# Kernel tuning notes

Hardware: AMD Instinct MI355X
Metric: run time of the kernel (lower is better)

## Reference

```python
import jax, jax.numpy as jnp
import numpy as np

EPS = 1e-7  # K.epsilon()


def setup_inputs() -> dict:
    key = jax.random.key(0)
    k1, k2, k3 = jax.random.split(key, 3)
    B, T, D = 32, 2048, 1024
    one = jax.random.normal(k1, (B, D), dtype=jnp.float32)
    many = jax.random.normal(k2, (B, T, D), dtype=jnp.float32)
    W = jax.random.normal(k3, (D, D), dtype=jnp.float32) * (1.0 / np.sqrt(D))
    return {"one": one, "many": many, "W": W}


def reference(one, many, W):
    # logits = batch_dot(tanh(many @ W), one, axes=[2,1]) -> [B, T]
    proj = jnp.tanh(jnp.einsum('btd,de->bte', many, W))       # [B,T,D]
    logits = jnp.einsum('btd,bd->bt', proj, one)               # [B,T]
    # stable softmax with Keras epsilon in denominator
    ai = jnp.exp(logits - jnp.max(logits, axis=-1, keepdims=True))
    att_weights = ai / (jnp.sum(ai, axis=-1, keepdims=True) + EPS)  # [B,T]
    result = jnp.einsum('btd,bt->bd', many, att_weights)       # [B,D]
    return result, att_weights
```

## Files before the change

kernel.cpp:

```cpp
#include <hip/hip_runtime.h>
#include <hip/hip_bf16.h>

typedef _Float16 half8v __attribute__((ext_vector_type(8)));
typedef __fp16  fp16x2 __attribute__((ext_vector_type(2)));
typedef float floatx4 __attribute__((ext_vector_type(4)));

#define NB 32
#define NT 2048
#define ND 1024
#define NM (NB * NT)

#define GL16(g, l)                                                             \
    __builtin_amdgcn_global_load_lds(                                          \
        (const __attribute__((address_space(1))) void*)(g),                    \
        (__attribute__((address_space(3))) void*)(l), 16, 0, 0)

__device__ __forceinline__ float fast_tanh(float x) {
    x = fminf(9.0f, fmaxf(-9.0f, x));
    float e = __builtin_amdgcn_exp2f(x * 2.8853900817779268f);
    return (e - 1.0f) * __builtin_amdgcn_rcpf(e + 1.0f);
}

__global__ __launch_bounds__(256)
void wt_kernel(const float* __restrict__ W, _Float16* __restrict__ Wt) {
    __shared__ float tile[32][33];
    int tx = threadIdx.x, ty = threadIdx.y;
    int bx = blockIdx.x, by = blockIdx.y;
    #pragma unroll
    for (int i = 0; i < 4; ++i) {
        int y = by * 32 + ty + i * 8;
        tile[ty + i * 8][tx] = W[y * ND + bx * 32 + tx];
    }
    __syncthreads();
    #pragma unroll
    for (int i = 0; i < 4; ++i) {
        int e = bx * 32 + ty + i * 8;
        Wt[e * ND + by * 32 + tx] = (_Float16)tile[tx][ty + i * 8];
    }
}

__global__ __launch_bounds__(256)
void conv_kernel(const float* __restrict__ many, _Float16* __restrict__ manyh) {
    size_t idx = ((size_t)blockIdx.x * 256 + threadIdx.x) * 8;
    size_t stride = (size_t)gridDim.x * 256 * 8;
    for (size_t i = idx; i < (size_t)NM * ND; i += stride) {
        float4 a = *reinterpret_cast<const float4*>(many + i);
        float4 b = *reinterpret_cast<const float4*>(many + i + 4);
        union { _Float16 h[8]; uint4 u; } o;
        o.h[0] = (_Float16)a.x; o.h[1] = (_Float16)a.y;
        o.h[2] = (_Float16)a.z; o.h[3] = (_Float16)a.w;
        o.h[4] = (_Float16)b.x; o.h[5] = (_Float16)b.y;
        o.h[6] = (_Float16)b.z; o.h[7] = (_Float16)b.w;
        *reinterpret_cast<uint4*>(manyh + i) = o.u;
    }
}

__global__ __launch_bounds__(512, 2)
void gemm_logits_8p(const _Float16* __restrict__ manyh, const _Float16* __restrict__ Wt,
                    const float* __restrict__ one, float* __restrict__ logits) {
    __shared__ uint4 LDSQ[8192];
    char* Ld = (char*)LDSQ;

    int bid = blockIdx.x;
    int j = (bid & 7) * 128 + (bid >> 3);
    int mb = j >> 2, nb = j & 3;
    int m0 = mb * 256, n0 = nb * 256;

    int tid = threadIdx.x;
    int lane = tid & 63, w = tid >> 6;
    int wr = w >> 2, wc = w & 3;
    int l15 = lane & 15, l4 = lane >> 4;

    const char* aS = (const char*)manyh + ((size_t)(m0 + (tid >> 3)) << 11)
                   + (size_t)(((tid & 7) ^ ((tid >> 3) & 7)) << 4);
    const char* bS = (const char*)Wt + ((size_t)(n0 + (tid >> 3)) << 11)
                   + (size_t)(((tid & 7) ^ ((tid >> 3) & 7)) << 4);
    int ldst = tid * 16;

#define SU(OP, H, L, TT)                                                        \
    GL16(((OP) ? bS : aS) + (((size_t)((H) * 128 + (L) * 64)) << 11) + (TT) * 128, \
         Ld + (((TT) & 1) << 16) + ((OP) << 15) + ((H) << 14) + ((L) << 13) + ldst)

    floatx4 acc[8][4] = {};
    int key = l15 & 7;
    int lofA0 = l15 * 128 + (((0 | l4) ^ key) << 4);
    int lofA1 = l15 * 128 + (((4 | l4) ^ key) << 4);

    SU(0, 0, 0, 0); SU(0, 1, 0, 0);
    SU(0, 0, 1, 0); SU(0, 1, 1, 0);
    SU(1, 0, 0, 0); SU(1, 0, 1, 0);
    SU(1, 1, 0, 0); SU(1, 1, 1, 0);
    SU(0, 0, 0, 1); SU(0, 1, 0, 1);
    asm volatile("s_waitcnt vmcnt(2)" ::: "memory");
    __builtin_amdgcn_sched_barrier(0);
    __builtin_amdgcn_s_barrier();

    #pragma unroll 1
    for (int t = 0; t < 16; ++t) {
        const char* ab = Ld + ((t & 1) << 16) + (wr << 14);
        const char* bb = Ld + ((t & 1) << 16) + 32768 + ((wc >> 1) << 14)
                       + ((wc & 1) << 13);
        half8v bf0[4], bf1[4];
        #pragma unroll
        for (int p = 0; p < 4; ++p) {
            int rb = (p * 32) << 7;
            half8v a0k0 = *(const half8v*)(ab + rb + lofA0);
            half8v a0k1 = *(const half8v*)(ab + rb + lofA1);
            half8v a1k0 = *(const half8v*)(ab + rb + (16 << 7) + lofA0);
            half8v a1k1 = *(const half8v*)(ab + rb + (16 << 7) + lofA1);
            if (p == 0) {
                #pragma unroll
                for (int ni = 0; ni < 4; ++ni) {
                    bf0[ni] = *(const half8v*)(bb + ((ni * 16) << 7) + lofA0);
                    bf1[ni] = *(const half8v*)(bb + ((ni * 16) << 7) + lofA1);
                }
            }
            if (t < 15) {
                if (p == 0)      { SU(0, 0, 1, t + 1); SU(0, 1, 1, t + 1); }
                else if (p == 1) { SU(1, 0, 0, t + 1); SU(1, 0, 1, t + 1); }
                else if (p == 2) { SU(1, 1, 0, t + 1); SU(1, 1, 1, t + 1); }
                else if (t < 14) { SU(0, 0, 0, t + 2); SU(0, 1, 0, t + 2); }
            }
            __builtin_amdgcn_s_barrier();
            __builtin_amdgcn_s_setprio(1);
            #pragma unroll
            for (int ni = 0; ni < 4; ++ni) {
                acc[2 * p][ni] = __builtin_amdgcn_mfma_f32_16x16x32_f16(
                    a0k0, bf0[ni], acc[2 * p][ni], 0, 0, 0);
                acc[2 * p][ni] = __builtin_amdgcn_mfma_f32_16x16x32_f16(
                    a0k1, bf1[ni], acc[2 * p][ni], 0, 0, 0);
                acc[2 * p + 1][ni] = __builtin_amdgcn_mfma_f32_16x16x32_f16(
                    a1k0, bf0[ni], acc[2 * p + 1][ni], 0, 0, 0);
                acc[2 * p + 1][ni] = __builtin_amdgcn_mfma_f32_16x16x32_f16(
                    a1k1, bf1[ni], acc[2 * p + 1][ni], 0, 0, 0);
            }
            __builtin_amdgcn_s_setprio(0);
            if (p == 3) {
                if (t < 14)       asm volatile("s_waitcnt vmcnt(2)" ::: "memory");
                else if (t == 14) asm volatile("s_waitcnt vmcnt(0)" ::: "memory");
                __builtin_amdgcn_sched_barrier(0);
            }
            __builtin_amdgcn_s_barrier();
        }
    }
#undef SU

    int bidx = m0 >> 11;
    float onev[4];
    #pragma unroll
    for (int ni = 0; ni < 4; ++ni)
        onev[ni] = one[(bidx << 10) + n0 + wc * 64 + ni * 16 + l15];

    #pragma unroll
    for (int mi = 0; mi < 8; ++mi) {
        float part[4] = {0.f, 0.f, 0.f, 0.f};
        #pragma unroll
        for (int ni = 0; ni < 4; ++ni)
            #pragma unroll
            for (int b = 0; b < 4; ++b)
                part[b] += fast_tanh(acc[mi][ni][b]) * onev[ni];
        #pragma unroll
        for (int off = 1; off < 16; off <<= 1)
            #pragma unroll
            for (int b = 0; b < 4; ++b)
                part[b] += __shfl_xor(part[b], off, 64);
        #pragma unroll
        for (int b = 0; b < 4; ++b)
            if (l15 == ((mi * 4 + b) & 15))
                atomicAdd(&logits[m0 + wr * 128 + mi * 16 + l4 * 4 + b], part[b]);
    }
}

__global__ __launch_bounds__(256, 2)
void gemm_logits(const float* __restrict__ many, const _Float16* __restrict__ Wt,
                 const float* __restrict__ one, float* __restrict__ logits) {
    __shared__ uint4 AsQ[2048];
    __shared__ uint4 BsQ[1024];
    char* AsB = (char*)AsQ;
    char* BsB = (char*)BsQ;

    int bid = blockIdx.x;
    int j = (bid & 7) * 512 + (bid >> 3);
    int mb = j >> 3, nb = j & 7;
    int m0 = mb * 128, n0 = nb * 128;

    int tid = threadIdx.x;
    int lane = tid & 63, w = tid >> 6;
    int wr = w >> 1, wc = w & 1;
    int l15 = lane & 15, l4 = lane >> 4;

    const char* aS = (const char*)many + ((size_t)(m0 + (tid >> 4)) << 12)
        + (size_t)(((tid & 15) ^ ((tid >> 4) & 7)) << 4);
    const char* bS = (const char*)Wt + ((size_t)(n0 + (tid >> 3)) << 11)
        + (size_t)(((tid & 7) ^ ((tid >> 3) & 7)) << 4);
    char* aD = AsB + tid * 16;
    char* bD = BsB + tid * 16;

    floatx4 acc[4][4] = {};

    for (int kb = 0; kb < 1024; kb += 64) {
        #pragma unroll
        for (int i = 0; i < 8; ++i)
            GL16(aS + kb * 4 + i * 65536, aD + i * 4096);
        #pragma unroll
        for (int i = 0; i < 4; ++i)
            GL16(bS + kb * 2 + i * 65536, bD + i * 4096);
        __syncthreads();

        #pragma unroll
        for (int ks = 0; ks < 64; ks += 32) {
            half8v af[4], bf[4];
            #pragma unroll
            for (int mi = 0; mi < 4; ++mi) {
                int r = wr * 64 + mi * 16 + l15;
                int s = l15 & 7;
                const char* base = AsB + r * 256;
                int c0 = (ks >> 2) + l4 * 2;
                float4 x = *(const float4*)(base + (size_t)((c0 ^ s) << 4));
                float4 y = *(const float4*)(base + (size_t)(((c0 + 1) ^ s) << 4));
                union { fp16x2 p[4]; half8v h; } u;
                u.p[0] = __builtin_amdgcn_cvt_pkrtz(x.x, x.y);
                u.p[1] = __builtin_amdgcn_cvt_pkrtz(x.z, x.w);
                u.p[2] = __builtin_amdgcn_cvt_pkrtz(y.x, y.y);
                u.p[3] = __builtin_amdgcn_cvt_pkrtz(y.z, y.w);
                af[mi] = u.h;
            }
            #pragma unroll
            for (int ni = 0; ni < 4; ++ni) {
                int r = wc * 64 + ni * 16 + l15;
                int s = l15 & 7;
                int c = (ks >> 3) + l4;
                bf[ni] = *(const half8v*)(BsB + r * 128 + (size_t)((c ^ s) << 4));
            }
            #pragma unroll
            for (int mi = 0; mi < 4; ++mi)
                #pragma unroll
                for (int ni = 0; ni < 4; ++ni)
                    acc[mi][ni] = __builtin_amdgcn_mfma_f32_16x16x32_f16(
                        af[mi], bf[ni], acc[mi][ni], 0, 0, 0);
        }
        __syncthreads();
    }

    int bidx = m0 >> 11;
    float onev[4];
    #pragma unroll
    for (int ni = 0; ni < 4; ++ni)
        onev[ni] = one[(bidx << 10) + n0 + wc * 64 + ni * 16 + l15];

    #pragma unroll
    for (int mi = 0; mi < 4; ++mi) {
        float part[4] = {0.f, 0.f, 0.f, 0.f};
        #pragma unroll
        for (int ni = 0; ni < 4; ++ni)
            #pragma unroll
            for (int b = 0; b < 4; ++b)
                part[b] += fast_tanh(acc[mi][ni][b]) * onev[ni];
        #pragma unroll
        for (int off = 1; off < 16; off <<= 1)
            #pragma unroll
            for (int b = 0; b < 4; ++b)
                part[b] += __shfl_xor(part[b], off, 64);
        #pragma unroll
        for (int b = 0; b < 4; ++b)
            if (l15 == mi * 4 + b)
                atomicAdd(&logits[m0 + wr * 64 + mi * 16 + l4 * 4 + b], part[b]);
    }
}

__global__ __launch_bounds__(256)
void softmax_kernel(const float* __restrict__ logits, float* __restrict__ att) {
    int b = blockIdx.x, tid = threadIdx.x;
    const float* lr = logits + (b << 11);
    float lv[8];
    float mx = -1e30f;
    #pragma unroll
    for (int i = 0; i < 8; ++i) { lv[i] = lr[tid + (i << 8)]; mx = fmaxf(mx, lv[i]); }
    #pragma unroll
    for (int off = 1; off < 64; off <<= 1) mx = fmaxf(mx, __shfl_xor(mx, off, 64));
    __shared__ float redm[4];
    __shared__ float reds[4];
    int wv = tid >> 6;
    if ((tid & 63) == 0) redm[wv] = mx;
    __syncthreads();
    mx = fmaxf(fmaxf(redm[0], redm[1]), fmaxf(redm[2], redm[3]));
    float s = 0.f;
    #pragma unroll
    for (int i = 0; i < 8; ++i) { lv[i] = expf(lv[i] - mx); s += lv[i]; }
    #pragma unroll
    for (int off = 1; off < 64; off <<= 1) s += __shfl_xor(s, off, 64);
    if ((tid & 63) == 0) reds[wv] = s;
    __syncthreads();
    s = reds[0] + reds[1] + reds[2] + reds[3];
    float inv = 1.0f / (s + 1e-7f);
    #pragma unroll
    for (int i = 0; i < 8; ++i) att[(b << 11) + tid + (i << 8)] = lv[i] * inv;
}

__global__ __launch_bounds__(256)
void out_kernel_h(const _Float16* __restrict__ manyh, const float* __restrict__ att,
                  float* __restrict__ out) {
    int b = blockIdx.x >> 4, tch = blockIdx.x & 15;
    int tid = threadIdx.x;
    __shared__ float aw[128];
    if (tid < 128) aw[tid] = att[(b << 11) + tch * 128 + tid];
    __syncthreads();
    const _Float16* mp = manyh + (((size_t)b * NT + tch * 128) << 10) + tid * 4;
    float a0 = 0.f, a1 = 0.f, a2 = 0.f, a3 = 0.f;
    for (int t = 0; t < 128; ++t) {
        float wgt = aw[t];
        union { _Float16 h[4]; uint2 u; } v;
        v.u = *reinterpret_cast<const uint2*>(mp + ((size_t)t << 10));
        a0 = fmaf((float)v.h[0], wgt, a0); a1 = fmaf((float)v.h[1], wgt, a1);
        a2 = fmaf((float)v.h[2], wgt, a2); a3 = fmaf((float)v.h[3], wgt, a3);
    }
    float* op = out + (b << 10) + tid * 4;
    atomicAdd(op + 0, a0); atomicAdd(op + 1, a1);
    atomicAdd(op + 2, a2); atomicAdd(op + 3, a3);
}

__global__ __launch_bounds__(256)
void out_kernel(const float* __restrict__ many, const float* __restrict__ att,
                float* __restrict__ out) {
    int b = blockIdx.x >> 4, tch = blockIdx.x & 15;
    int tid = threadIdx.x;
    __shared__ float aw[128];
    if (tid < 128) aw[tid] = att[(b << 11) + tch * 128 + tid];
    __syncthreads();
    const float* mp = many + (((size_t)b * NT + tch * 128) << 10) + tid * 4;
    float ax = 0.f, ay = 0.f, az = 0.f, aww = 0.f;
    for (int t = 0; t < 128; ++t) {
        float wgt = aw[t];
        float4 v = *reinterpret_cast<const float4*>(mp + ((size_t)t << 10));
        ax = fmaf(v.x, wgt, ax); ay = fmaf(v.y, wgt, ay);
        az = fmaf(v.z, wgt, az); aww = fmaf(v.w, wgt, aww);
    }
    float* op = out + (b << 10) + tid * 4;
    atomicAdd(op + 0, ax); atomicAdd(op + 1, ay);
    atomicAdd(op + 2, az); atomicAdd(op + 3, aww);
}

extern "C" void kernel_launch(void* const* d_in, const int* in_sizes, int n_in,
                              void* d_out, int out_size, void* d_ws, size_t ws_size,
                              hipStream_t stream) {
    const float* one  = (const float*)d_in[0];
    const float* many = (const float*)d_in[1];
    const float* W    = (const float*)d_in[2];
    float* out = (float*)d_out;

    size_t wtB = (size_t)ND * ND * 2;
    size_t lgB = (size_t)NM * 4;
    size_t mhB = (size_t)NM * ND * 2;
    _Float16* Wt    = (_Float16*)d_ws;
    float*    logits = (float*)((char*)d_ws + wtB);
    _Float16* manyh = (_Float16*)((char*)d_ws + wtB + lgB);
    float*    att   = out + NB * ND;
    bool big = ws_size >= wtB + lgB + mhB;

    (void)hipMemsetAsync(out, 0, (size_t)NB * ND * sizeof(float), stream);
    (void)hipMemsetAsync(logits, 0, (size_t)NM * sizeof(float), stream);

    wt_kernel<<<dim3(32, 32), dim3(32, 8), 0, stream>>>(W, Wt);
    if (big) {
        conv_kernel<<<2048, 256, 0, stream>>>(many, manyh);
        gemm_logits_8p<<<1024, 512, 0, stream>>>(manyh, Wt, one, logits);
    } else {
        gemm_logits<<<4096, 256, 0, stream>>>(many, Wt, one, logits);
    }
    softmax_kernel<<<NB, 256, 0, stream>>>(logits, att);
    if (big) out_kernel_h<<<NB * 16, 256, 0, stream>>>(manyh, att, out);
    else     out_kernel<<<NB * 16, 256, 0, stream>>>(many, att, out);
}
```

Before: 272.8 us.

## Rework GEMM main loop into ten-slot LDS ring with quadrant-phased MFMA

```diff
diff --git a/kernel.cpp b/kernel.cpp
--- a/kernel.cpp
+++ b/kernel.cpp
@@ -56,9 +56,9 @@
 }
 
 __global__ __launch_bounds__(512, 2)
-void gemm_logits_8p(const _Float16* __restrict__ manyh, const _Float16* __restrict__ Wt,
-                    const float* __restrict__ one, float* __restrict__ logits) {
-    __shared__ uint4 LDSQ[8192];
+void gemm_logits_10s(const _Float16* __restrict__ manyh, const _Float16* __restrict__ Wt,
+                     const float* __restrict__ one, float* __restrict__ logits) {
+    __shared__ uint4 LDSQ[10240];
     char* Ld = (char*)LDSQ;
 
     int bid = blockIdx.x;
@@ -77,73 +77,87 @@
                    + (size_t)(((tid & 7) ^ ((tid >> 3) & 7)) << 4);
     int ldst = tid * 16;
 
-#define SU(OP, H, L, TT)                                                        \
-    GL16(((OP) ? bS : aS) + (((size_t)((H) * 128 + (L) * 64)) << 11) + (TT) * 128, \
-         Ld + (((TT) & 1) << 16) + ((OP) << 15) + ((H) << 14) + ((L) << 13) + ldst)
+#define SUNIT(u) do {                                                          \
+        int r_ = (u) & 3, tt_ = (u) >> 2, sl_ = (u) % 10;                      \
+        const char* s_ = ((r_ >> 1) ? bS : aS) + ((size_t)(r_ & 1) << 18)      \
+                         + ((size_t)tt_ << 7);                                 \
+        char* d_ = Ld + sl_ * 16384 + ldst;                                    \
+        GL16(s_, d_);                                                          \
+        GL16(s_ + (64u << 11), d_ + 8192);                                     \
+    } while (0)
 
     floatx4 acc[8][4] = {};
     int key = l15 & 7;
-    int lofA0 = l15 * 128 + (((0 | l4) ^ key) << 4);
-    int lofA1 = l15 * 128 + (((4 | l4) ^ key) << 4);
-
-    SU(0, 0, 0, 0); SU(0, 1, 0, 0);
-    SU(0, 0, 1, 0); SU(0, 1, 1, 0);
-    SU(1, 0, 0, 0); SU(1, 0, 1, 0);
-    SU(1, 1, 0, 0); SU(1, 1, 1, 0);
-    SU(0, 0, 0, 1); SU(0, 1, 0, 1);
-    asm volatile("s_waitcnt vmcnt(2)" ::: "memory");
+    int lof0 = l15 * 128 + (((0 | l4) ^ key) << 4);
+    int lof1 = l15 * 128 + (((4 | l4) ^ key) << 4);
+
+    #pragma unroll
+    for (int u = 0; u < 6; ++u) SUNIT(u);
+    asm volatile("s_waitcnt vmcnt(4)" ::: "memory");
     __builtin_amdgcn_sched_barrier(0);
     __builtin_amdgcn_s_barrier();
 
+    half8v af[4][2], b0f[2][2], b1f[2][2];
+
     #pragma unroll 1
     for (int t = 0; t < 16; ++t) {
-        const char* ab = Ld + ((t & 1) << 16) + (wr << 14);
-        const char* bb = Ld + ((t & 1) << 16) + 32768 + ((wc >> 1) << 14)
-                       + ((wc & 1) << 13);
-        half8v bf0[4], bf1[4];
-        #pragma unroll
-        for (int p = 0; p < 4; ++p) {
-            int rb = (p * 32) << 7;
-            half8v a0k0 = *(const half8v*)(ab + rb + lofA0);
-            half8v a0k1 = *(const half8v*)(ab + rb + lofA1);
-            half8v a1k0 = *(const half8v*)(ab + rb + (16 << 7) + lofA0);
-            half8v a1k1 = *(const half8v*)(ab + rb + (16 << 7) + lofA1);
-            if (p == 0) {
-                #pragma unroll
-                for (int ni = 0; ni < 4; ++ni) {
-                    bf0[ni] = *(const half8v*)(bb + ((ni * 16) << 7) + lofA0);
-                    bf1[ni] = *(const half8v*)(bb + ((ni * 16) << 7) + lofA1);
-                }
-            }
-            if (t < 15) {
-                if (p == 0)      { SU(0, 0, 1, t + 1); SU(0, 1, 1, t + 1); }
-                else if (p == 1) { SU(1, 0, 0, t + 1); SU(1, 0, 1, t + 1); }
-                else if (p == 2) { SU(1, 1, 0, t + 1); SU(1, 1, 1, t + 1); }
-                else if (t < 14) { SU(0, 0, 0, t + 2); SU(0, 1, 0, t + 2); }
-            }
-            __builtin_amdgcn_s_barrier();
-            __builtin_amdgcn_s_setprio(1);
-            #pragma unroll
-            for (int ni = 0; ni < 4; ++ni) {
-                acc[2 * p][ni] = __builtin_amdgcn_mfma_f32_16x16x32_f16(
-                    a0k0, bf0[ni], acc[2 * p][ni], 0, 0, 0);
-                acc[2 * p][ni] = __builtin_amdgcn_mfma_f32_16x16x32_f16(
-                    a0k1, bf1[ni], acc[2 * p][ni], 0, 0, 0);
-                acc[2 * p + 1][ni] = __builtin_amdgcn_mfma_f32_16x16x32_f16(
-                    a1k0, bf0[ni], acc[2 * p + 1][ni], 0, 0, 0);
-                acc[2 * p + 1][ni] = __builtin_amdgcn_mfma_f32_16x16x32_f16(
-                    a1k1, bf1[ni], acc[2 * p + 1][ni], 0, 0, 0);
-            }
-            __builtin_amdgcn_s_setprio(0);
-            if (p == 3) {
-                if (t < 14)       asm volatile("s_waitcnt vmcnt(2)" ::: "memory");
-                else if (t == 14) asm volatile("s_waitcnt vmcnt(0)" ::: "memory");
-                __builtin_amdgcn_sched_barrier(0);
-            }
-            __builtin_amdgcn_s_barrier();
-        }
-    }
-#undef SU
+        int t4 = t * 4;
+        const char* ab = Ld + ((t4 + wr) % 10) * 16384;
+        const char* bb = Ld + ((t4 + 2 + (wc >> 1)) % 10) * 16384 + ((wc & 1) << 13);
+
+#define PHASE(Q) do {                                                          \
+        constexpr int qm_ = (Q) >> 1;                                          \
+        if ((Q) == 0 || (Q) == 2) {                                            \
+            _Pragma("unroll")                                                  \
+            for (int mi = 0; mi < 4; ++mi) {                                   \
+                af[mi][0] = *(const half8v*)(ab + (qm_ << 13) + (mi << 11) + lof0); \
+                af[mi][1] = *(const half8v*)(ab + (qm_ << 13) + (mi << 11) + lof1); \
+            }                                                                  \
+        }                                                                      \
+        if ((Q) == 0) {                                                        \
+            _Pragma("unroll")                                                  \
+            for (int ni = 0; ni < 2; ++ni) {                                   \
+                b0f[ni][0] = *(const half8v*)(bb + (ni << 11) + lof0);         \
+                b0f[ni][1] = *(const half8v*)(bb + (ni << 11) + lof1);         \
+            }                                                                  \
+        }                                                                      \
+        if ((Q) == 1) {                                                        \
+            _Pragma("unroll")                                                  \
+            for (int ni = 0; ni < 2; ++ni) {                                   \
+                b1f[ni][0] = *(const half8v*)(bb + 4096 + (ni << 11) + lof0);  \
+                b1f[ni][1] = *(const half8v*)(bb + 4096 + (ni << 11) + lof1);  \
+            }                                                                  \
+        }                                                                      \
+        { int u_ = t4 + 6 + (Q); if (u_ <= 63) SUNIT(u_); }                    \
+        __builtin_amdgcn_s_barrier();                                          \
+        __builtin_amdgcn_s_setprio(1);                                         \
+        _Pragma("unroll")                                                      \
+        for (int kk = 0; kk < 2; ++kk)                                         \
+            _Pragma("unroll")                                                  \
+            for (int mi = 0; mi < 4; ++mi)                                     \
+                _Pragma("unroll")                                              \
+                for (int ni = 0; ni < 2; ++ni)                                 \
+                    acc[qm_ * 4 + mi][((Q) & 1) * 2 + ni] =                    \
+                        __builtin_amdgcn_mfma_f32_16x16x32_f16(                \
+                            af[mi][kk], ((Q) & 1) ? b1f[ni][kk] : b0f[ni][kk], \
+                            acc[qm_ * 4 + mi][((Q) & 1) * 2 + ni], 0, 0, 0);   \
+        __builtin_amdgcn_s_setprio(0);                                         \
+    } while (0)
+
+        PHASE(0);
+        __builtin_amdgcn_s_barrier();
+        PHASE(1);
+        __builtin_amdgcn_s_barrier();
+        PHASE(2);
+        __builtin_amdgcn_s_barrier();
+        PHASE(3);
+        if (t <= 13)      asm volatile("s_waitcnt vmcnt(4)" ::: "memory");
+        else if (t == 14) asm volatile("s_waitcnt vmcnt(0)" ::: "memory");
+        __builtin_amdgcn_sched_barrier(0);
+        __builtin_amdgcn_s_barrier();
+#undef PHASE
+    }
+#undef SUNIT
 
     int bidx = m0 >> 11;
     float onev[4];
@@ -363,7 +377,7 @@
     wt_kernel<<<dim3(32, 32), dim3(32, 8), 0, stream>>>(W, Wt);
     if (big) {
         conv_kernel<<<2048, 256, 0, stream>>>(many, manyh);
-        gemm_logits_8p<<<1024, 512, 0, stream>>>(manyh, Wt, one, logits);
+        gemm_logits_10s<<<1024, 512, 0, stream>>>(manyh, Wt, one, logits);
     } else {
         gemm_logits<<<4096, 256, 0, stream>>>(many, Wt, one, logits);
     }
```

Measured after the change: 276.3 us. About the same (+1.3%).
